# Kernel tuning notes

Hardware: AMD Instinct MI355X
Metric: run time of the kernel (lower is better)

The kernel has to match this reference:

```python
import jax, jax.numpy as jnp
import numpy as np

B, S, D, H = 2, 2048, 1024, 16
HD = D // H  # 64


def setup_inputs() -> dict:
    key = jax.random.key(0)
    ks = jax.random.split(key, 6)
    x = jax.random.normal(ks[0], (B, S, D), dtype=jnp.float32)
    # rotary frequencies: theta = 10000^{-2i/hd}, angles = pos * theta
    inv_freq = 1.0 / (10000.0 ** (jnp.arange(0, HD, 2, dtype=jnp.float32) / HD))  # [HD/2]
    angles = jnp.arange(S, dtype=jnp.float32)[:, None] * inv_freq[None, :]  # [S, HD/2]
    freqs_cos = jnp.cos(angles)
    freqs_sin = jnp.sin(angles)
    scale = 0.02
    w_qkv = jax.random.normal(ks[1], (3 * D, D), dtype=jnp.float32) * scale
    b_qkv = jnp.zeros((3 * D,), dtype=jnp.float32)
    w_dense = jax.random.normal(ks[2], (D, D), dtype=jnp.float32) * scale
    b_dense = jnp.zeros((D,), dtype=jnp.float32)
    return {"x": x, "w_qkv": w_qkv, "b_qkv": b_qkv, "w_dense": w_dense,
            "b_dense": b_dense, "freqs_cos": freqs_cos, "freqs_sin": freqs_sin}


def _apply_rope(t, cos, sin):
    # t: [B, S, H, HD]; cos/sin: [S, HD/2] broadcast as [1, S, 1, HD/2]
    tr = t.reshape(t.shape[:-1] + (HD // 2, 2))
    x0, x1 = tr[..., 0], tr[..., 1]
    c = cos[None, :, None, :]
    s = sin[None, :, None, :]
    o0 = x0 * c - x1 * s  # real part of complex multiply
    o1 = x0 * s + x1 * c  # imag part
    return jnp.stack([o0, o1], axis=-1).reshape(t.shape)


def reference(x, w_qkv, b_qkv, w_dense, b_dense, freqs_cos, freqs_sin):
    b, s, d = x.shape
    qkv = x @ w_qkv.T + b_qkv              # [B, S, 3D]
    qkv = qkv.reshape(b, s, 3, H, HD)
    q, k, v = qkv[:, :, 0], qkv[:, :, 1], qkv[:, :, 2]  # [B, S, H, HD]
    q = _apply_rope(q, freqs_cos, freqs_sin)
    k = _apply_rope(k, freqs_cos, freqs_sin)
    # causal SDPA, scale = 1/sqrt(head_dim)
    q = q.transpose(0, 2, 1, 3)  # [B, H, S, HD]
    k = k.transpose(0, 2, 1, 3)
    v = v.transpose(0, 2, 1, 3)
    scores = jnp.einsum('bhqd,bhkd->bhqk', q, k) / jnp.sqrt(jnp.float32(HD))
    causal = jnp.tril(jnp.ones((s, s), dtype=bool))
    scores = jnp.where(causal[None, None], scores, jnp.finfo(scores.dtype).min)
    attn = jax.nn.softmax(scores, axis=-1)
    ctx = jnp.einsum('bhqk,bhkd->bhqd', attn, v)   # [B, H, S, HD]
    ctx = ctx.transpose(0, 2, 1, 3).reshape(b, s, d)
    return ctx @ w_dense.T + b_dense
```

## Files before the change

kernel.cpp:

```cpp
#include <hip/hip_runtime.h>
#include <stdint.h>

#define Bb 2
#define Ss 2048
#define Dd 1024
#define Hh 16
#define HDd 64

typedef float f32x4 __attribute__((ext_vector_type(4)));
typedef __bf16 bf16x8 __attribute__((ext_vector_type(8)));
typedef __bf16 bf16x2 __attribute__((ext_vector_type(2)));
typedef short s16x8 __attribute__((ext_vector_type(8)));

__device__ inline unsigned short f2bf(float f) {
  unsigned u = __builtin_bit_cast(unsigned, f);
  u += 0x7fffu + ((u >> 16) & 1u);
  return (unsigned short)(u >> 16);
}
__device__ inline float bf2f(unsigned short h) {
  unsigned u = ((unsigned)h) << 16;
  return __builtin_bit_cast(float, u);
}
__device__ inline unsigned pkcvt(float a, float b) {
  bf16x2 v;
  v[0] = (__bf16)a;
  v[1] = (__bf16)b;
  return __builtin_bit_cast(unsigned, v);
}
__device__ inline float ex2(float x) {
#if __has_builtin(__builtin_amdgcn_exp2f)
  return __builtin_amdgcn_exp2f(x);
#else
  float r;
  asm("v_exp_f32 %0, %1\n\ts_nop 1" : "=v"(r) : "v"(x));
  return r;
#endif
}
__device__ inline int swz(int row, int soff) {
  return (row << 6) + ((((soff >> 3) ^ (row & 7)) << 3) | (soff & 7));
}

#define GLDS(dst, src)                                                        \
  __builtin_amdgcn_global_load_lds(                                           \
      (const __attribute__((address_space(1))) void*)(src),                   \
      (__attribute__((address_space(3))) void*)(dst), 16, 0, 0)

__global__ void cast_all(const float* __restrict__ x, const float* __restrict__ wq,
                         const float* __restrict__ wd, unsigned short* __restrict__ dst) {
  int i = blockIdx.x * blockDim.x + threadIdx.x;
  float4 v;
  if (i < 1048576) v = ((const float4*)x)[i];
  else if (i < 1835008) v = ((const float4*)wq)[i - 1048576];
  else v = ((const float4*)wd)[i - 1835008];
  ushort4 o;
  o.x = f2bf(v.x); o.y = f2bf(v.y); o.z = f2bf(v.z); o.w = f2bf(v.w);
  ((ushort4*)dst)[i] = o;
}

template <int MODE>
__global__ __launch_bounds__(512, 2) void gemm256(
    const unsigned short* __restrict__ A, const unsigned short* __restrict__ Bw,
    const float* __restrict__ bias, void* __restrict__ Cout,
    unsigned short* __restrict__ vtout,
    const float* __restrict__ fc, const float* __restrict__ fs,
    int M, int N, int K, int NT) {
  __shared__ __align__(16) unsigned short Asl[2][2][256 * 32];
  __shared__ __align__(16) unsigned short Bsl[2][2][256 * 32];
  const int tid = threadIdx.x;
  const int w = tid >> 6, l = tid & 63;
  const int lg = l >> 4, lr = l & 15;
  const int wm = w >> 2, wn = w & 3;
  int id = blockIdx.y * gridDim.x + blockIdx.x;
  const int nwg = gridDim.x * gridDim.y;
  id = (id & 7) * (nwg >> 3) + (id >> 3);
  const int bx = id % gridDim.x, by = id / gridDim.x;
  const int mbase = by * 256, nbase = bx * 192;

  const int r0 = w * 16 + (l >> 2);
  const int r1 = r0 + 128;
  const int sp = l & 3;
  const unsigned short* a0 = A + (size_t)(mbase + r0) * K + (sp ^ ((r0 >> 1) & 3)) * 8;
  const unsigned short* a1 = A + (size_t)(mbase + r1) * K + (sp ^ ((r1 >> 1) & 3)) * 8;
  const unsigned short* b0 = Bw + (size_t)(nbase + r0) * K + (sp ^ ((r0 >> 1) & 3)) * 8;
  const unsigned short* b1 = Bw + (size_t)(nbase + r1) * K + (sp ^ ((r1 >> 1) & 3)) * 8;
  const int d0 = w * 512 + l * 8;
  const int d1 = d0 + 4096;

  GLDS(&Bsl[0][0][d0], b0);      GLDS(&Bsl[0][0][d1], b1);
  GLDS(&Asl[0][0][d0], a0);      GLDS(&Asl[0][0][d1], a1);
  GLDS(&Bsl[0][1][d0], b0 + 32); GLDS(&Bsl[0][1][d1], b1 + 32);
  GLDS(&Asl[0][1][d0], a0 + 32); GLDS(&Asl[0][1][d1], a1 + 32);

  f32x4 acc[8][3] = {};
  for (int t = 0; t < NT; ++t) {
    const int cur = t & 1, nxt = cur ^ 1;
    const int kN = (t + 1) * 64;
    bf16x8 bfr[3], af[4];
    asm volatile("s_waitcnt vmcnt(4)" ::: "memory");
    __builtin_amdgcn_s_barrier();
    asm volatile("" ::: "memory");
#pragma unroll
    for (int ni = 0; ni < 3; ++ni) {
      int row = wn * 48 + ni * 16 + lr;
      bfr[ni] = *(const bf16x8*)(&Bsl[cur][0][row * 32 + ((lg ^ ((row >> 1) & 3)) << 3)]);
    }
#pragma unroll
    for (int j = 0; j < 4; ++j) {
      int row = wm * 128 + j * 16 + lr;
      af[j] = *(const bf16x8*)(&Asl[cur][0][row * 32 + ((lg ^ ((row >> 1) & 3)) << 3)]);
    }
    if (t + 1 < NT) { GLDS(&Bsl[nxt][0][d0], b0 + kN); GLDS(&Bsl[nxt][0][d1], b1 + kN); }
    __builtin_amdgcn_s_setprio(1);
#pragma unroll
    for (int j = 0; j < 4; ++j)
#pragma unroll
      for (int ni = 0; ni < 3; ++ni)
        acc[j][ni] = __builtin_amdgcn_mfma_f32_16x16x32_bf16(af[j], bfr[ni], acc[j][ni], 0, 0, 0);
    __builtin_amdgcn_s_setprio(0);
#pragma unroll
    for (int j = 0; j < 4; ++j) {
      int row = wm * 128 + (j + 4) * 16 + lr;
      af[j] = *(const bf16x8*)(&Asl[cur][0][row * 32 + ((lg ^ ((row >> 1) & 3)) << 3)]);
    }
    if (t + 1 < NT) { GLDS(&Asl[nxt][0][d0], a0 + kN); GLDS(&Asl[nxt][0][d1], a1 + kN); }
    __builtin_amdgcn_s_setprio(1);
#pragma unroll
    for (int j = 0; j < 4; ++j)
#pragma unroll
      for (int ni = 0; ni < 3; ++ni)
        acc[j + 4][ni] = __builtin_amdgcn_mfma_f32_16x16x32_bf16(af[j], bfr[ni], acc[j + 4][ni], 0, 0, 0);
    __builtin_amdgcn_s_setprio(0);
    if (t + 1 < NT) asm volatile("s_waitcnt vmcnt(4)" ::: "memory");
    else            asm volatile("s_waitcnt vmcnt(0)" ::: "memory");
    __builtin_amdgcn_s_barrier();
    asm volatile("" ::: "memory");
#pragma unroll
    for (int ni = 0; ni < 3; ++ni) {
      int row = wn * 48 + ni * 16 + lr;
      bfr[ni] = *(const bf16x8*)(&Bsl[cur][1][row * 32 + ((lg ^ ((row >> 1) & 3)) << 3)]);
    }
#pragma unroll
    for (int j = 0; j < 4; ++j) {
      int row = wm * 128 + j * 16 + lr;
      af[j] = *(const bf16x8*)(&Asl[cur][1][row * 32 + ((lg ^ ((row >> 1) & 3)) << 3)]);
    }
    if (t + 1 < NT) { GLDS(&Asl[nxt][1][d0], a0 + kN + 32); GLDS(&Asl[nxt][1][d1], a1 + kN + 32); }
    __builtin_amdgcn_s_setprio(1);
#pragma unroll
    for (int j = 0; j < 4; ++j)
#pragma unroll
      for (int ni = 0; ni < 3; ++ni)
        acc[j][ni] = __builtin_amdgcn_mfma_f32_16x16x32_bf16(af[j], bfr[ni], acc[j][ni], 0, 0, 0);
    __builtin_amdgcn_s_setprio(0);
#pragma unroll
    for (int j = 0; j < 4; ++j) {
      int row = wm * 128 + (j + 4) * 16 + lr;
      af[j] = *(const bf16x8*)(&Asl[cur][1][row * 32 + ((lg ^ ((row >> 1) & 3)) << 3)]);
    }
    if (t + 1 < NT) { GLDS(&Bsl[nxt][1][d0], b0 + kN + 32); GLDS(&Bsl[nxt][1][d1], b1 + kN + 32); }
    __builtin_amdgcn_s_setprio(1);
#pragma unroll
    for (int j = 0; j < 4; ++j)
#pragma unroll
      for (int ni = 0; ni < 3; ++ni)
        acc[j + 4][ni] = __builtin_amdgcn_mfma_f32_16x16x32_bf16(af[j], bfr[ni], acc[j + 4][ni], 0, 0, 0);
    __builtin_amdgcn_s_setprio(0);
  }

#pragma unroll
  for (int mi = 0; mi < 8; ++mi)
#pragma unroll
    for (int ni = 0; ni < 3; ++ni) {
      int col = nbase + wn * 48 + ni * 16 + lr;
      float bi = bias[col];
      int row0 = mbase + wm * 128 + mi * 16 + lg * 4;
      float o4[4];
#pragma unroll
      for (int r = 0; r < 4; ++r) o4[r] = acc[mi][ni][r] + bi;
      if constexpr (MODE == 0) {
#pragma unroll
        for (int r = 0; r < 4; ++r)
          ((float*)Cout)[(size_t)(row0 + r) * N + col] = o4[r];
      } else {
        int sect = col >> 10;
        int d = col & 63;
        int srow0 = row0 & 2047;
        if (sect < 2) {
          int p = d >> 1;
#pragma unroll
          for (int r = 0; r < 4; ++r) {
            float vp = __shfl_xor(o4[r], 1);
            float c = fc[(srow0 + r) * 32 + p];
            float s = fs[(srow0 + r) * 32 + p];
            float o = (d & 1) ? (vp * s + o4[r] * c) : (o4[r] * c - vp * s);
            ((unsigned short*)Cout)[(size_t)(row0 + r) * 3072 + col] = f2bf(o);
          }
        } else {
          int bh = (row0 >> 11) * 16 + ((col >> 6) & 15);
          uint2 o;
          o.x = pkcvt(o4[0], o4[1]);
          o.y = pkcvt(o4[2], o4[3]);
          *(uint2*)&vtout[((size_t)(bh * 64 + d)) * 2048 + srow0] = o;
        }
      }
    }
}

__global__ __launch_bounds__(256) void gemm_bt(
    const unsigned short* __restrict__ A, const unsigned short* __restrict__ Bw,
    const float* __restrict__ bias, float* __restrict__ Cout,
    int M, int N, int K) {
  __shared__ __align__(16) unsigned short As[128 * 32];
  __shared__ __align__(16) unsigned short Bs[128 * 32];
  const int tid = threadIdx.x;
  const int w = tid >> 6, l = tid & 63;
  const int lg = l >> 4, lr = l & 15;
  const int mbase = blockIdx.y * 128, nbase = blockIdx.x * 128;
  const int wr = w >> 1, wc = w & 1;
  f32x4 acc[4][4] = {};

  for (int k0 = 0; k0 < K; k0 += 32) {
#pragma unroll
    for (int r = 0; r < 2; ++r) {
      int c = r * 256 + w * 64 + l;
      int row = c >> 2, c8 = c & 3;
      GLDS(As + c * 8, A + (size_t)(mbase + row) * K + k0 + c8 * 8);
      GLDS(Bs + c * 8, Bw + (size_t)(nbase + row) * K + k0 + c8 * 8);
    }
    __syncthreads();
    bf16x8 af[4], bfr[4];
#pragma unroll
    for (int mi = 0; mi < 4; ++mi)
      af[mi] = *(const bf16x8*)(As + (wr * 64 + mi * 16 + lr) * 32 + lg * 8);
#pragma unroll
    for (int ni = 0; ni < 4; ++ni)
      bfr[ni] = *(const bf16x8*)(Bs + (wc * 64 + ni * 16 + lr) * 32 + lg * 8);
#pragma unroll
    for (int mi = 0; mi < 4; ++mi)
#pragma unroll
      for (int ni = 0; ni < 4; ++ni)
        acc[mi][ni] = __builtin_amdgcn_mfma_f32_16x16x32_bf16(
            af[mi], bfr[ni], acc[mi][ni], 0, 0, 0);
    __syncthreads();
  }

#pragma unroll
  for (int mi = 0; mi < 4; ++mi) {
#pragma unroll
    for (int ni = 0; ni < 4; ++ni) {
      int col = nbase + wc * 64 + ni * 16 + lr;
      float bi = bias[col];
#pragma unroll
      for (int r = 0; r < 4; ++r) {
        int row = mbase + wr * 64 + mi * 16 + lg * 4 + r;
        Cout[(size_t)row * N + col] = acc[mi][ni][r] + bi;
      }
    }
  }
}

__global__ __launch_bounds__(512, 4) void attn(
    const unsigned short* __restrict__ qkv, const unsigned short* __restrict__ vt,
    unsigned short* __restrict__ ctx) {
  __shared__ __align__(16) unsigned short Ks[2][64 * 64];
  __shared__ __align__(16) unsigned short Vs[2][64 * 64];
  __shared__ __align__(16) unsigned short Ps[8][16 * 64];
  int did = blockIdx.x;
  int x = did & 7, rest = did >> 3;
  int bh = x * 4 + (rest & 3);
  int qi = 31 - (rest >> 2);
  int b = bh >> 4, h = bh & 15;
  int qbase = qi * 64;
  int tid = threadIdx.x;
  int w = tid >> 6, l = tid & 63;
  int lg = l >> 4, lr = l & 15;
  int wq = w & 3, wk = w >> 2;

  bf16x8 qb[2];
#pragma unroll
  for (int kc = 0; kc < 2; ++kc) {
    s16x8 qr = *(const s16x8*)(qkv +
        (size_t)(b * Ss + qbase + wq * 16 + lr) * 3072 + h * 64 + kc * 32 + lg * 8);
    bf16x8 qs;
#pragma unroll
    for (int e = 0; e < 8; ++e)
      qs[e] = (__bf16)(bf2f((unsigned short)qr[e]) * 0.18033688f);
    qb[kc] = qs;
  }

  int tt = tid >> 8, rr = (tid >> 2) & 63, sc = (tid & 3) * 16;
  const unsigned short* kp =
      qkv + ((size_t)(b * Ss) + rr) * 3072 + 1024 + h * 64 + sc;
  const unsigned short* vp = vt + ((size_t)bh * 64 + rr) * 2048 + sc;

  int nkt = qi + 1;
  int nsup = (nkt + 1) >> 1;

  if (tt < nkt) {
    const unsigned short* gk = kp + (size_t)tt * 64 * 3072;
    const unsigned short* gv = vp + tt * 64;
    *(s16x8*)&Ks[tt][swz(rr, sc)]     = *(const s16x8*)gk;
    *(s16x8*)&Ks[tt][swz(rr, sc + 8)] = *(const s16x8*)(gk + 8);
    *(s16x8*)&Vs[tt][swz(rr, sc)]     = *(const s16x8*)gv;
    *(s16x8*)&Vs[tt][swz(rr, sc + 8)] = *(const s16x8*)(gv + 8);
  }
  s16x8 rk0, rk1, rv0, rv1;
  if (2 + tt < nkt) {
    const unsigned short* gk = kp + (size_t)(2 + tt) * 64 * 3072;
    const unsigned short* gv = vp + (2 + tt) * 64;
    rk0 = *(const s16x8*)gk;  rk1 = *(const s16x8*)(gk + 8);
    rv0 = *(const s16x8*)gv;  rv1 = *(const s16x8*)(gv + 8);
  }
  __syncthreads();

  f32x4 acc[4] = {};
  float mrow = -1e30f, lsum = 0.f;

  for (int j = 0; j < nsup; ++j) {
    int kt = 2 * j + wk;
    if (kt < nkt) {
      f32x4 st[4] = {};
      __builtin_amdgcn_s_setprio(1);
#pragma unroll
      for (int kc = 0; kc < 2; ++kc) {
#pragma unroll
        for (int ni = 0; ni < 4; ++ni) {
          bf16x8 ka = *(const bf16x8*)&Ks[wk][swz(ni * 16 + lr, kc * 32 + lg * 8)];
          st[ni] = __builtin_amdgcn_mfma_f32_16x16x32_bf16(ka, qb[kc], st[ni], 0, 0, 0);
        }
      }
      __builtin_amdgcn_s_setprio(0);

      float tm = -1e30f;
      if (kt == qi) {
        int rq = wq * 16 + lr;
#pragma unroll
        for (int ni = 0; ni < 4; ++ni)
#pragma unroll
          for (int r4 = 0; r4 < 4; ++r4) {
            float s = st[ni][r4];
            if (ni * 16 + lg * 4 + r4 > rq) s = -1e30f;
            st[ni][r4] = s;
            tm = fmaxf(tm, s);
          }
      } else {
#pragma unroll
        for (int ni = 0; ni < 4; ++ni)
#pragma unroll
          for (int r4 = 0; r4 < 4; ++r4) tm = fmaxf(tm, st[ni][r4]);
      }
      if (!__all(tm <= mrow + 8.0f)) {
        tm = fmaxf(tm, __shfl_xor(tm, 16));
        tm = fmaxf(tm, __shfl_xor(tm, 32));
        float mnew = fmaxf(mrow, tm);
        float alpha = ex2(mrow - mnew);
        lsum *= alpha;
#pragma unroll
        for (int nd = 0; nd < 4; ++nd)
#pragma unroll
          for (int r4 = 0; r4 < 4; ++r4) acc[nd][r4] *= alpha;
        mrow = mnew;
      }
      float sum = 0.f;
#pragma unroll
      for (int ni = 0; ni < 4; ++ni)
#pragma unroll
        for (int r4 = 0; r4 < 4; ++r4) {
          float pe = ex2(st[ni][r4] - mrow);
          st[ni][r4] = pe;
          sum += pe;
        }
      lsum += sum;
#pragma unroll
      for (int ni = 0; ni < 4; ++ni) {
        uint2 wv;
        wv.x = pkcvt(st[ni][0], st[ni][1]);
        wv.y = pkcvt(st[ni][2], st[ni][3]);
        *(uint2*)&Ps[w][swz(lr, ni * 16 + lg * 4)] = wv;
      }
      __builtin_amdgcn_s_setprio(1);
#pragma unroll
      for (int kc = 0; kc < 2; ++kc) {
        bf16x8 pbf = *(const bf16x8*)&Ps[w][swz(lr, kc * 32 + lg * 8)];
#pragma unroll
        for (int nd = 0; nd < 4; ++nd) {
          bf16x8 va = *(const bf16x8*)&Vs[wk][swz(nd * 16 + lr, kc * 32 + lg * 8)];
          acc[nd] = __builtin_amdgcn_mfma_f32_16x16x32_bf16(va, pbf, acc[nd], 0, 0, 0);
        }
      }
      __builtin_amdgcn_s_setprio(0);
    }

    if (j + 1 < nsup) {
      __syncthreads();
      int tw = 2 * (j + 1) + tt;
      if (tw < nkt) {
        *(s16x8*)&Ks[tt][swz(rr, sc)]     = rk0;
        *(s16x8*)&Ks[tt][swz(rr, sc + 8)] = rk1;
        *(s16x8*)&Vs[tt][swz(rr, sc)]     = rv0;
        *(s16x8*)&Vs[tt][swz(rr, sc + 8)] = rv1;
      }
      int tn = 2 * (j + 2) + tt;
      if (tn < nkt) {
        const unsigned short* gk = kp + (size_t)tn * 64 * 3072;
        const unsigned short* gv = vp + tn * 64;
        rk0 = *(const s16x8*)gk;  rk1 = *(const s16x8*)(gk + 8);
        rv0 = *(const s16x8*)gv;  rv1 = *(const s16x8*)(gv + 8);
      }
      __syncthreads();
    }
  }

  lsum += __shfl_xor(lsum, 16);
  lsum += __shfl_xor(lsum, 32);
  __syncthreads();
  float* accS = (float*)Vs;
  float* mlS  = (float*)Ks;
  if (wk == 1) {
    float* as = accS + (wq * 64 + l) * 16;
#pragma unroll
    for (int nd = 0; nd < 4; ++nd) *(f32x4*)(as + nd * 4) = acc[nd];
    mlS[(wq * 64 + l) * 2 + 0] = mrow;
    mlS[(wq * 64 + l) * 2 + 1] = lsum;
  }
  __syncthreads();
  if (wk == 0) {
    const float* as = accS + (wq * 64 + l) * 16;
    float m1 = mlS[(wq * 64 + l) * 2 + 0];
    float l1 = mlS[(wq * 64 + l) * 2 + 1];
    float M  = fmaxf(mrow, m1);
    float s0 = ex2(mrow - M), s1 = ex2(m1 - M);
    float inv = 1.0f / (lsum * s0 + l1 * s1);
    float f0 = s0 * inv, f1 = s1 * inv;
    int qg = qbase + wq * 16 + lr;
#pragma unroll
    for (int nd = 0; nd < 4; ++nd) {
      f32x4 a1 = *(const f32x4*)(as + nd * 4);
      uint2 o;
      o.x = pkcvt(acc[nd][0] * f0 + a1[0] * f1, acc[nd][1] * f0 + a1[1] * f1);
      o.y = pkcvt(acc[nd][2] * f0 + a1[2] * f1, acc[nd][3] * f0 + a1[3] * f1);
      *(uint2*)&ctx[((size_t)(b * Ss) + qg) * 1024 + h * 64 + nd * 16 + lg * 4] = o;
    }
  }
}

extern "C" void kernel_launch(void* const* d_in, const int* in_sizes, int n_in,
                              void* d_out, int out_size, void* d_ws, size_t ws_size,
                              hipStream_t stream) {
  const float* x       = (const float*)d_in[0];
  const float* w_qkv   = (const float*)d_in[1];
  const float* b_qkv   = (const float*)d_in[2];
  const float* w_dense = (const float*)d_in[3];
  const float* b_dense = (const float*)d_in[4];
  const float* fc      = (const float*)d_in[5];
  const float* fs      = (const float*)d_in[6];
  float* out = (float*)d_out;

  char* ws = (char*)d_ws;
  unsigned short* xb    = (unsigned short*)(ws);
  unsigned short* wqkvb = (unsigned short*)(ws + (8ull  << 20));
  unsigned short* wdb   = (unsigned short*)(ws + (14ull << 20));
  unsigned short* qkvb  = (unsigned short*)(ws + (16ull << 20));
  unsigned short* vt    = (unsigned short*)(ws + (40ull << 20));

  cast_all<<<8192, 256, 0, stream>>>(x, w_qkv, w_dense, xb);

  gemm256<2><<<dim3(16, 16), 512, 0, stream>>>(xb, wqkvb, b_qkv, qkvb, vt,
                                               fc, fs, 4096, 3072, 1024, 16);
  attn<<<1024, 512, 0, stream>>>(qkvb, vt, xb );
  gemm_bt<<<dim3(8, 32), 256, 0, stream>>>(xb, wdb, b_dense, out,
                                           4096, 1024, 1024);
}
```

Measured before the change: 112.6 us.

## Software-pipeline LDS fragment reads with register double buffering in GEMM loop

Restructures the GEMM main loop so LDS fragment reads for the next MFMA group are issued while the current group computes, using two register sets for A and B fragments. The first fragments of the next K tile are loaded before the loop iteration ends. Barriers drop from two to one inside the iteration, plus one at the tail, and the vmcnt waits are retuned to match the new order of global-to-LDS prefetches. The goal is to hide LDS latency and barrier stalls behind MFMA work. The cost is higher register pressure and a tighter dependence on the exact order of asynchronous loads and waits.

Result: no change. 112.7 us (+0.1%).

```diff
diff --git a/kernel.cpp b/kernel.cpp
--- a/kernel.cpp
+++ b/kernel.cpp
@@ -86,86 +86,74 @@
   const int d0 = w * 512 + l * 8;
   const int d1 = d0 + 4096;
 
+#define RD_B(dst, buf, half)                                                  \
+  _Pragma("unroll")                                                           \
+  for (int ni = 0; ni < 3; ++ni) {                                            \
+    int row = wn * 48 + ni * 16 + lr;                                         \
+    dst[ni] = *(const bf16x8*)(&Bsl[buf][half][row * 32 +                     \
+                  ((lg ^ ((row >> 1) & 3)) << 3)]);                           \
+  }
+#define RD_A(dst, buf, half, hh)                                              \
+  _Pragma("unroll")                                                           \
+  for (int j = 0; j < 4; ++j) {                                               \
+    int row = wm * 128 + (j + (hh) * 4) * 16 + lr;                            \
+    dst[j] = *(const bf16x8*)(&Asl[buf][half][row * 32 +                      \
+                  ((lg ^ ((row >> 1) & 3)) << 3)]);                           \
+  }
+#define MFMA12(afv, bfv, off)                                                 \
+  __builtin_amdgcn_s_setprio(1);                                              \
+  _Pragma("unroll")                                                           \
+  for (int j = 0; j < 4; ++j)                                                 \
+    _Pragma("unroll")                                                         \
+    for (int ni = 0; ni < 3; ++ni)                                            \
+      acc[j + (off)][ni] = __builtin_amdgcn_mfma_f32_16x16x32_bf16(           \
+          afv[j], bfv[ni], acc[j + (off)][ni], 0, 0, 0);                      \
+  __builtin_amdgcn_s_setprio(0);
+
   GLDS(&Bsl[0][0][d0], b0);      GLDS(&Bsl[0][0][d1], b1);
   GLDS(&Asl[0][0][d0], a0);      GLDS(&Asl[0][0][d1], a1);
   GLDS(&Bsl[0][1][d0], b0 + 32); GLDS(&Bsl[0][1][d1], b1 + 32);
   GLDS(&Asl[0][1][d0], a0 + 32); GLDS(&Asl[0][1][d1], a1 + 32);
+  asm volatile("s_waitcnt vmcnt(4)" ::: "memory");
+  __builtin_amdgcn_s_barrier();
+  asm volatile("" ::: "memory");
+
+  bf16x8 bfr0[3], bfr1[3], af0[4], af1[4];
+  RD_B(bfr0, 0, 0);
+  RD_A(af0, 0, 0, 0);
 
   f32x4 acc[8][3] = {};
   for (int t = 0; t < NT; ++t) {
     const int cur = t & 1, nxt = cur ^ 1;
     const int kN = (t + 1) * 64;
-    bf16x8 bfr[3], af[4];
-    asm volatile("s_waitcnt vmcnt(4)" ::: "memory");
+    const bool pf = (t + 1 < NT);
+    RD_A(af1, cur, 0, 1);
+    if (pf) { GLDS(&Bsl[nxt][0][d0], b0 + kN); GLDS(&Bsl[nxt][0][d1], b1 + kN); }
+    MFMA12(af0, bfr0, 0);
+    if (pf) asm volatile("s_waitcnt vmcnt(2)" ::: "memory");
+    else    asm volatile("s_waitcnt vmcnt(0)" ::: "memory");
     __builtin_amdgcn_s_barrier();
     asm volatile("" ::: "memory");
-#pragma unroll
-    for (int ni = 0; ni < 3; ++ni) {
-      int row = wn * 48 + ni * 16 + lr;
-      bfr[ni] = *(const bf16x8*)(&Bsl[cur][0][row * 32 + ((lg ^ ((row >> 1) & 3)) << 3)]);
-    }
-#pragma unroll
-    for (int j = 0; j < 4; ++j) {
-      int row = wm * 128 + j * 16 + lr;
-      af[j] = *(const bf16x8*)(&Asl[cur][0][row * 32 + ((lg ^ ((row >> 1) & 3)) << 3)]);
-    }
-    if (t + 1 < NT) { GLDS(&Bsl[nxt][0][d0], b0 + kN); GLDS(&Bsl[nxt][0][d1], b1 + kN); }
-    __builtin_amdgcn_s_setprio(1);
-#pragma unroll
-    for (int j = 0; j < 4; ++j)
-#pragma unroll
-      for (int ni = 0; ni < 3; ++ni)
-        acc[j][ni] = __builtin_amdgcn_mfma_f32_16x16x32_bf16(af[j], bfr[ni], acc[j][ni], 0, 0, 0);
-    __builtin_amdgcn_s_setprio(0);
-#pragma unroll
-    for (int j = 0; j < 4; ++j) {
-      int row = wm * 128 + (j + 4) * 16 + lr;
-      af[j] = *(const bf16x8*)(&Asl[cur][0][row * 32 + ((lg ^ ((row >> 1) & 3)) << 3)]);
-    }
-    if (t + 1 < NT) { GLDS(&Asl[nxt][0][d0], a0 + kN); GLDS(&Asl[nxt][0][d1], a1 + kN); }
-    __builtin_amdgcn_s_setprio(1);
-#pragma unroll
-    for (int j = 0; j < 4; ++j)
-#pragma unroll
-      for (int ni = 0; ni < 3; ++ni)
-        acc[j + 4][ni] = __builtin_amdgcn_mfma_f32_16x16x32_bf16(af[j], bfr[ni], acc[j + 4][ni], 0, 0, 0);
-    __builtin_amdgcn_s_setprio(0);
-    if (t + 1 < NT) asm volatile("s_waitcnt vmcnt(4)" ::: "memory");
-    else            asm volatile("s_waitcnt vmcnt(0)" ::: "memory");
-    __builtin_amdgcn_s_barrier();
-    asm volatile("" ::: "memory");
-#pragma unroll
-    for (int ni = 0; ni < 3; ++ni) {
-      int row = wn * 48 + ni * 16 + lr;
-      bfr[ni] = *(const bf16x8*)(&Bsl[cur][1][row * 32 + ((lg ^ ((row >> 1) & 3)) << 3)]);
-    }
-#pragma unroll
-    for (int j = 0; j < 4; ++j) {
-      int row = wm * 128 + j * 16 + lr;
-      af[j] = *(const bf16x8*)(&Asl[cur][1][row * 32 + ((lg ^ ((row >> 1) & 3)) << 3)]);
-    }
-    if (t + 1 < NT) { GLDS(&Asl[nxt][1][d0], a0 + kN + 32); GLDS(&Asl[nxt][1][d1], a1 + kN + 32); }
-    __builtin_amdgcn_s_setprio(1);
-#pragma unroll
-    for (int j = 0; j < 4; ++j)
-#pragma unroll
-      for (int ni = 0; ni < 3; ++ni)
-        acc[j][ni] = __builtin_amdgcn_mfma_f32_16x16x32_bf16(af[j], bfr[ni], acc[j][ni], 0, 0, 0);
-    __builtin_amdgcn_s_setprio(0);
-#pragma unroll
-    for (int j = 0; j < 4; ++j) {
-      int row = wm * 128 + (j + 4) * 16 + lr;
-      af[j] = *(const bf16x8*)(&Asl[cur][1][row * 32 + ((lg ^ ((row >> 1) & 3)) << 3)]);
-    }
-    if (t + 1 < NT) { GLDS(&Bsl[nxt][1][d0], b0 + kN + 32); GLDS(&Bsl[nxt][1][d1], b1 + kN + 32); }
-    __builtin_amdgcn_s_setprio(1);
-#pragma unroll
-    for (int j = 0; j < 4; ++j)
-#pragma unroll
-      for (int ni = 0; ni < 3; ++ni)
-        acc[j + 4][ni] = __builtin_amdgcn_mfma_f32_16x16x32_bf16(af[j], bfr[ni], acc[j + 4][ni], 0, 0, 0);
-    __builtin_amdgcn_s_setprio(0);
-  }
+    RD_B(bfr1, cur, 1);
+    RD_A(af0, cur, 1, 0);
+    if (pf) { GLDS(&Asl[nxt][0][d0], a0 + kN); GLDS(&Asl[nxt][0][d1], a1 + kN); }
+    MFMA12(af1, bfr0, 4);
+    RD_A(af1, cur, 1, 1);
+    if (pf) { GLDS(&Bsl[nxt][1][d0], b0 + kN + 32); GLDS(&Bsl[nxt][1][d1], b1 + kN + 32); }
+    MFMA12(af0, bfr1, 0);
+    if (pf) { GLDS(&Asl[nxt][1][d0], a0 + kN + 32); GLDS(&Asl[nxt][1][d1], a1 + kN + 32); }
+    MFMA12(af1, bfr1, 4);
+    if (pf) {
+      asm volatile("s_waitcnt vmcnt(4)" ::: "memory");
+      __builtin_amdgcn_s_barrier();
+      asm volatile("" ::: "memory");
+      RD_B(bfr0, nxt, 0);
+      RD_A(af0, nxt, 0, 0);
+    }
+  }
+#undef RD_B
+#undef RD_A
+#undef MFMA12
 
 #pragma unroll
   for (int mi = 0; mi < 8; ++mi)
```
